# Optimization experiments

Hardware: AMD Instinct MI355X
Metric: run time of the kernel (lower is better)

## Reference

```python
import jax, jax.numpy as jnp
import numpy as np

B, T, D_MODEL, HEAD = 4, 4096, 1024, 64

def setup_inputs() -> dict:
    key = jax.random.key(0)
    ks = jax.random.split(key, 7)
    s = 0.02  # typical init scale
    return {
        "x":  jax.random.normal(ks[0], (B, T, D_MODEL), dtype=jnp.float32),
        "Wq": jax.random.normal(ks[1], (D_MODEL, HEAD), dtype=jnp.float32) * s,
        "bq": jnp.zeros((HEAD,), dtype=jnp.float32),
        "Wk": jax.random.normal(ks[2], (D_MODEL, HEAD), dtype=jnp.float32) * s,
        "bk": jnp.zeros((HEAD,), dtype=jnp.float32),
        "Wv": jax.random.normal(ks[3], (D_MODEL, HEAD), dtype=jnp.float32) * s,
        "bv": jnp.zeros((HEAD,), dtype=jnp.float32),
    }

def reference(x, Wq, bq, Wk, bk, Wv, bv):
    Bz, Tz, C = x.shape
    q = x @ Wq + bq                      # (B,T,H)
    k = x @ Wk + bk                      # (B,T,H)
    v = x @ Wv + bv                      # (B,T,H)
    # NOTE: original scales by sqrt(C) = sqrt(d_model), not sqrt(head_size)
    att = jnp.einsum("bth,bsh->bts", q, k) / jnp.sqrt(jnp.float32(C))
    causal = jnp.tril(jnp.ones((Tz, Tz), dtype=bool))
    att = jnp.where(causal, att, -jnp.inf)
    att = jax.nn.softmax(att, axis=-1)
    return jnp.einsum("bts,bsh->bth", att, v)  # (B,T,H)
```

## Files before the change

### kernel.cpp

```cpp
#include <hip/hip_runtime.h>
#include <hip/hip_bf16.h>
#include <hip/hip_fp16.h>

#define T_SEQ 4096
#define DMODEL 1024
#define HEAD 64
#define NBATCH 4
#define NSEG 544
#define S2LOG 0.04508422f

typedef __attribute__((ext_vector_type(8))) short bf16x8;
typedef __attribute__((ext_vector_type(4))) float f32x4;

__device__ __forceinline__ unsigned short f2bf(float f) {
    unsigned int b = __float_as_uint(f);
    unsigned int r = b + 0x7FFFu + ((b >> 16) & 1u);
    return (unsigned short)(r >> 16);
}
__device__ __forceinline__ unsigned int pk_bf16(float a, float b) {
    __hip_bfloat162 h = __float22bfloat162_rn(make_float2(a, b));
    unsigned int u; __builtin_memcpy(&u, &h, 4); return u;
}
__device__ __forceinline__ void dma16(const void* g, void* s) {
    __builtin_amdgcn_global_load_lds(
        (const __attribute__((address_space(1))) unsigned int*)g,
        (__attribute__((address_space(3))) unsigned int*)s, 16, 0, 0);
}

__global__ __launch_bounds__(256) void prep_w(
    const float* __restrict__ Wq, const float* __restrict__ Wk,
    const float* __restrict__ Wv, unsigned short* __restrict__ Wtb)
{
    __shared__ unsigned short tl[64 * 72];
    const int bid = blockIdx.x;
    const int m   = bid >> 4;
    const int k0  = (bid & 15) * 64;
    const float* W = (m == 0) ? Wq : (m == 1) ? Wk : Wv;
    const int t  = threadIdx.x;
    const int kr = t >> 2, qtr = t & 3;
#pragma unroll
    for (int i = 0; i < 4; ++i) {
        float4 wv4 = *(const float4*)&W[(k0 + kr) * 64 + qtr * 16 + i * 4];
        tl[(qtr * 16 + i * 4 + 0) * 72 + kr] = f2bf(wv4.x);
        tl[(qtr * 16 + i * 4 + 1) * 72 + kr] = f2bf(wv4.y);
        tl[(qtr * 16 + i * 4 + 2) * 72 + kr] = f2bf(wv4.z);
        tl[(qtr * 16 + i * 4 + 3) * 72 + kr] = f2bf(wv4.w);
    }
    __syncthreads();
#pragma unroll
    for (int c = 0; c < 2; ++c) {
        const int lin = c * 256 + t;
        const int n = lin >> 3, k8 = lin & 7;
        *(uint4*)&Wtb[((long)(m * 64 + n)) * 1024 + k0 + k8 * 8] =
            *(const uint4*)&tl[n * 72 + k8 * 8];
    }
}

__global__ __launch_bounds__(256, 3) void qkv_mfma(
    const float* __restrict__ x, const unsigned short* __restrict__ Wtb,
    const float* __restrict__ bq, const float* __restrict__ bk,
    const float* __restrict__ bv,
    unsigned short* __restrict__ qo, unsigned short* __restrict__ ko,
    unsigned short* __restrict__ vt)
{
    __shared__ __align__(16) unsigned short xs[2][4096];
    const int t    = threadIdx.x;
    const int lane = t & 63;
    const int l15  = lane & 15, quad = lane >> 4;
    const int w    = __builtin_amdgcn_readfirstlane(t >> 6);
    const long row0 = (long)blockIdx.x * 32;

    float bias[3];
#pragma unroll
    for (int ntl = 0; ntl < 3; ++ntl) {
        const int c = w * 48 + ntl * 16 + l15;
        bias[ntl] = (c < 64) ? bq[c] : (c < 128) ? bk[c - 64] : bv[c - 128];
    }
    f32x4 acc[2][3];
#pragma unroll
    for (int mt = 0; mt < 2; ++mt)
#pragma unroll
        for (int ntl = 0; ntl < 3; ++ntl)
            acc[mt][ntl] = (f32x4){bias[ntl], bias[ntl], bias[ntl], bias[ntl]};

    float4 g[4];
    auto load_stage = [&](int sg) {
#pragma unroll
        for (int s = 0; s < 4; ++s) {
            const int id = s * 256 + t, row = id >> 5, off = id & 31;
            g[s] = *(const float4*)&x[(row0 + row) * DMODEL + sg * 128 + off * 4];
        }
    };
    auto write_stage = [&](int buf) {
#pragma unroll
        for (int s = 0; s < 4; ++s) {
            const int id = s * 256 + t, row = id >> 5, off = id & 31;
            uint2 u;
            u.x = pk_bf16(g[s].x, g[s].y);
            u.y = pk_bf16(g[s].z, g[s].w);
            *(uint2*)&xs[buf][row * 128 + ((off >> 1) ^ (row & 7)) * 8 + (off & 1) * 4] = u;
        }
    };

    load_stage(0);
    write_stage(0);

    for (int sg = 0; sg < 8; ++sg) {
        __syncthreads();
        if (sg + 1 < 8) load_stage(sg + 1);
        bf16x8 wf[3][4];
#pragma unroll
        for (int ntl = 0; ntl < 3; ++ntl)
#pragma unroll
            for (int kq = 0; kq < 4; ++kq)
                wf[ntl][kq] = *(const bf16x8*)&Wtb[((long)(w * 48 + ntl * 16 + l15)) * 1024
                                                   + sg * 128 + kq * 32 + quad * 8];
#pragma unroll
        for (int mt = 0; mt < 2; ++mt)
#pragma unroll
            for (int kq = 0; kq < 4; ++kq) {
                const int row = mt * 16 + l15;
                bf16x8 a = *(const bf16x8*)&xs[sg & 1][row * 128
                                                       + ((kq * 4 + quad) ^ (row & 7)) * 8];
#pragma unroll
                for (int ntl = 0; ntl < 3; ++ntl)
                    acc[mt][ntl] = __builtin_amdgcn_mfma_f32_16x16x32_bf16(a, wf[ntl][kq], acc[mt][ntl], 0, 0, 0);
            }
        if (sg + 1 < 8) write_stage((sg + 1) & 1);
    }
#pragma unroll
    for (int mt = 0; mt < 2; ++mt)
#pragma unroll
        for (int ntl = 0; ntl < 3; ++ntl) {
            const int c = w * 48 + ntl * 16 + l15;
            const long tr0 = row0 + mt * 16 + quad * 4;
            if (c < 64) {
#pragma unroll
                for (int r = 0; r < 4; ++r)
                    qo[(tr0 + r) * HEAD + c] = f2bf(acc[mt][ntl][r] * S2LOG);
            } else if (c < 128) {
#pragma unroll
                for (int r = 0; r < 4; ++r)
                    ko[(tr0 + r) * HEAD + (c - 64)] = f2bf(acc[mt][ntl][r]);
            } else {
                const int b = (int)(tr0 >> 12), tloc = (int)(tr0 & 4095);
                uint2 pv;
                pv.x = pk_bf16(acc[mt][ntl][0], acc[mt][ntl][1]);
                pv.y = pk_bf16(acc[mt][ntl][2], acc[mt][ntl][3]);
                *(uint2*)&vt[((long)(b * HEAD + (c - 128))) * T_SEQ + tloc] = pv;
            }
        }
}

__global__ __launch_bounds__(256, 3) void flash_seg(
    const unsigned short* __restrict__ qg,
    const unsigned short* __restrict__ kg,
    const unsigned short* __restrict__ vtg,
    __half* __restrict__ opart, float* __restrict__ ml)
{
    __shared__ __align__(16) unsigned short kv_s[2][8192];
    __shared__ __align__(16) unsigned short p_s[4][16 * 72];
    const int t0   = threadIdx.x;
    const int lane = t0 & 63;
    const int l15  = lane & 15, quad = lane >> 4;
    const int wv   = __builtin_amdgcn_readfirstlane(t0 >> 6);

    const int bid = (int)blockIdx.x;
    const int sid = (NSEG - 1) - (bid >> 2);
    const int b   = bid & 3;

    int kk = 0, pref = 0;
#pragma unroll
    for (int i = 0; i < 15; ++i) {
        const int cnt = 4 * (kk + 1);
        if (sid >= pref + cnt) { pref += cnt; ++kk; }
    }
    const int S   = kk + 1;
    const int rem = sid - pref;
    const int t   = kk * 4 + rem / S;
    const int si  = rem % S;
    const int r0  = t * 64;
    const int rw  = r0 + wv * 16;
    const int nck = t + 1;
    const int c0  = (si * nck) / S, c1 = ((si + 1) * nck) / S;
    const long bbase = (long)b * T_SEQ;
    const int gidx = b * NSEG + sid;

    bf16x8 qf[2];
#pragma unroll
    for (int h = 0; h < 2; ++h)
        qf[h] = *(const bf16x8*)&qg[(bbase + rw + l15) * HEAD + h * 32 + quad * 8];

    f32x4 o[4];
#pragma unroll
    for (int dt = 0; dt < 4; ++dt) o[dt] = (f32x4){0.f, 0.f, 0.f, 0.f};
    float lrun = 0.f;
    unsigned short* ps = p_s[wv];

    auto dma_chunk = [&](int key0, int buf) {
#pragma unroll
        for (int i = 0; i < 2; ++i) {
            const int jj  = wv * 2 + i;
            const int kl  = jj * 8 + (lane >> 3);
            const int dlg = (lane & 7) ^ ((lane >> 3) & 7);
            dma16(kg + (bbase + key0 + kl) * HEAD + dlg * 8,
                  &kv_s[buf][jj * 512]);
        }
#pragma unroll
        for (int i = 0; i < 2; ++i) {
            const int jj  = wv * 2 + i;
            const int dim = jj * 8 + (lane >> 3);
            const int klg = (lane & 7) ^ ((lane >> 3) & 7);
            dma16(vtg + ((long)(b * HEAD + dim)) * T_SEQ + key0 + klg * 8,
                  &kv_s[buf][4096 + jj * 512]);
        }
    };
    dma_chunk(c0 * 64, 0);

    for (int c = c0; c < c1; ++c) {
        const int key0 = c * 64;
        const int cur  = (c - c0) & 1;
        __syncthreads();
        if (c + 1 < c1) dma_chunk((c + 1) * 64, cur ^ 1);

        f32x4 st[4];
#pragma unroll
        for (int mt = 0; mt < 4; ++mt) {
            const int key_l = mt * 16 + l15;
            bf16x8 k0 = *(const bf16x8*)&kv_s[cur][key_l * 64 + ((quad    ) ^ (l15 & 7)) * 8];
            bf16x8 k1 = *(const bf16x8*)&kv_s[cur][key_l * 64 + ((quad + 4) ^ (l15 & 7)) * 8];
            f32x4 z = (f32x4){0.f, 0.f, 0.f, 0.f};
            z = __builtin_amdgcn_mfma_f32_16x16x32_bf16(k0, qf[0], z, 0, 0, 0);
            st[mt] = __builtin_amdgcn_mfma_f32_16x16x32_bf16(k1, qf[1], st[mt] = z, 0, 0, 0);
        }
        bf16x8 vf[4][2];
#pragma unroll
        for (int dt = 0; dt < 4; ++dt) {
            const int dim = dt * 16 + l15;
            vf[dt][0] = *(const bf16x8*)&kv_s[cur][4096 + dim * 64 + ((quad    ) ^ (l15 & 7)) * 8];
            vf[dt][1] = *(const bf16x8*)&kv_s[cur][4096 + dim * 64 + ((quad + 4) ^ (l15 & 7)) * 8];
        }
        if (key0 + 63 > rw) {
            const int row = rw + l15;
#pragma unroll
            for (int mt = 0; mt < 4; ++mt)
#pragma unroll
                for (int r = 0; r < 4; ++r) {
                    const int key = key0 + mt * 16 + quad * 4 + r;
                    st[mt][r] = (key <= row) ? st[mt][r] : -30000.f;
                }
        }
        float psum = 0.f;
#pragma unroll
        for (int mt = 0; mt < 4; ++mt) {
            float e0 = exp2f(st[mt][0]), e1 = exp2f(st[mt][1]);
            float e2 = exp2f(st[mt][2]), e3 = exp2f(st[mt][3]);
            psum += (e0 + e1) + (e2 + e3);
            *(unsigned int*)&ps[l15 * 72 + mt * 16 + quad * 4]     = pk_bf16(e0, e1);
            *(unsigned int*)&ps[l15 * 72 + mt * 16 + quad * 4 + 2] = pk_bf16(e2, e3);
        }
        psum += __shfl_xor(psum, 16);
        psum += __shfl_xor(psum, 32);
        lrun += psum;
        __builtin_amdgcn_wave_barrier();
        bf16x8 pf[2];
#pragma unroll
        for (int g = 0; g < 2; ++g)
            pf[g] = *(const bf16x8*)&ps[l15 * 72 + g * 32 + quad * 8];
        __builtin_amdgcn_wave_barrier();
#pragma unroll
        for (int dt = 0; dt < 4; ++dt) {
            o[dt] = __builtin_amdgcn_mfma_f32_16x16x32_bf16(vf[dt][0], pf[0], o[dt], 0, 0, 0);
            o[dt] = __builtin_amdgcn_mfma_f32_16x16x32_bf16(vf[dt][1], pf[1], o[dt], 0, 0, 0);
        }
    }

    const float inv = (lrun > 0.f) ? 1.f / lrun : 0.f;
    __half* op = opart + (long)gidx * 4096;
#pragma unroll
    for (int dt = 0; dt < 4; ++dt) {
        __half2 h0 = __floats2half2_rn(o[dt][0] * inv, o[dt][1] * inv);
        __half2 h1 = __floats2half2_rn(o[dt][2] * inv, o[dt][3] * inv);
        uint2 u; __builtin_memcpy(&u.x, &h0, 4); __builtin_memcpy(&u.y, &h1, 4);
        *(uint2*)&op[(wv * 16 + l15) * HEAD + dt * 16 + quad * 4] = u;
    }
    if (quad == 0)
        ml[(long)gidx * 64 + wv * 16 + l15] = lrun;
}

__global__ __launch_bounds__(256) void merge_seg(
    const __half* __restrict__ opart, const float* __restrict__ ml,
    float* __restrict__ out)
{
    const int bid = blockIdx.x;
    const int half = bid & 1, t = (bid >> 1) & 63, b = bid >> 7;
    const int kk = t >> 2, S = kk + 1;
    const int base_sid = 2 * kk * (kk + 1) + (t & 3) * S;
    const int tid = threadIdx.x;
    const int row = half * 32 + (tid >> 3), col0 = (tid & 7) * 8;

    float acc[8];
#pragma unroll
    for (int j = 0; j < 8; ++j) acc[j] = 0.f;
    float L = 0.f;
    for (int si = 0; si < S; ++si) {
        const long g = (long)(b * NSEG + base_sid + si);
        const float l = ml[g * 64 + row];
        L += l;
        const __half* op = opart + g * 4096 + row * 64 + col0;
        uint4 u = *(const uint4*)op;
        __half2 h01, h23, h45, h67;
        __builtin_memcpy(&h01, &u.x, 4); __builtin_memcpy(&h23, &u.y, 4);
        __builtin_memcpy(&h45, &u.z, 4); __builtin_memcpy(&h67, &u.w, 4);
        float2 f01 = __half22float2(h01), f23 = __half22float2(h23);
        float2 f45 = __half22float2(h45), f67 = __half22float2(h67);
        acc[0] += l * f01.x; acc[1] += l * f01.y;
        acc[2] += l * f23.x; acc[3] += l * f23.y;
        acc[4] += l * f45.x; acc[5] += l * f45.y;
        acc[6] += l * f67.x; acc[7] += l * f67.y;
    }
    const float inv = 1.f / L;
    float* dst = out + ((long)(b * T_SEQ + t * 64 + row)) * HEAD + col0;
#pragma unroll
    for (int h = 0; h < 2; ++h) {
        float4 ov = {acc[h * 4] * inv, acc[h * 4 + 1] * inv,
                     acc[h * 4 + 2] * inv, acc[h * 4 + 3] * inv};
        *(float4*)(dst + h * 4) = ov;
    }
}

extern "C" void kernel_launch(void* const* d_in, const int* in_sizes, int n_in,
                              void* d_out, int out_size, void* d_ws, size_t ws_size,
                              hipStream_t stream) {
    const float* x  = (const float*)d_in[0];
    const float* Wq = (const float*)d_in[1];
    const float* bq = (const float*)d_in[2];
    const float* Wk = (const float*)d_in[3];
    const float* bk = (const float*)d_in[4];
    const float* Wv = (const float*)d_in[5];
    const float* bv = (const float*)d_in[6];
    float* outp = (float*)d_out;

    char* wsb = (char*)d_ws;
    unsigned short* wtb = (unsigned short*)(wsb);
    unsigned short* qw  = (unsigned short*)(wsb + 393216);
    unsigned short* kw  = (unsigned short*)(wsb + 2490368);
    unsigned short* vtw = (unsigned short*)(wsb + 4587520);
    __half* opart       = (__half*)(wsb + 6684672);
    float*  mlp         = (float*)(wsb + 24510464);

    prep_w<<<dim3(48), dim3(256), 0, stream>>>(Wq, Wk, Wv, wtb);
    qkv_mfma<<<dim3(512), dim3(256), 0, stream>>>(
        x, wtb, bq, bk, bv, qw, kw, vtw);
    flash_seg<<<dim3(NSEG * NBATCH), dim3(256), 0, stream>>>(qw, kw, vtw, opart, mlp);
    merge_seg<<<dim3(512), dim3(256), 0, stream>>>(opart, mlp, outp);
}
```

Measured before the change: 157.6 us.

## Stage QKV weights in LDS via async DMA and double rows per block

The projection kernel now processes 64 rows per block with 8 waves (two row groups by four column groups), so each weight tile is reused across twice as many rows. Weights are re-laid out per 128-wide k-stage and prefetched into double-buffered, swizzled LDS with global_load_lds instead of each wave reading them straight from global memory. This targets redundant global or L2 weight traffic in the QKV GEMM. In exchange it uses much more LDS per block (about 128 KB) and halves the grid to 256 blocks, which may lower occupancy.

```diff
diff --git a/kernel.cpp b/kernel.cpp
--- a/kernel.cpp
+++ b/kernel.cpp
@@ -51,29 +51,34 @@
     for (int c = 0; c < 2; ++c) {
         const int lin = c * 256 + t;
         const int n = lin >> 3, k8 = lin & 7;
-        *(uint4*)&Wtb[((long)(m * 64 + n)) * 1024 + k0 + k8 * 8] =
+        const int k = k0 + k8 * 8;
+        const int sg = k >> 7, koff = k & 127;
+        *(uint4*)&Wtb[((long)(sg * 192 + m * 64 + n)) * 128 + koff] =
             *(const uint4*)&tl[n * 72 + k8 * 8];
     }
 }
 
-__global__ __launch_bounds__(256, 3) void qkv_mfma(
+__global__ __launch_bounds__(512, 2) void qkv_mfma(
     const float* __restrict__ x, const unsigned short* __restrict__ Wtb,
     const float* __restrict__ bq, const float* __restrict__ bk,
     const float* __restrict__ bv,
     unsigned short* __restrict__ qo, unsigned short* __restrict__ ko,
     unsigned short* __restrict__ vt)
 {
-    __shared__ __align__(16) unsigned short xs[2][4096];
+    __shared__ __align__(16) unsigned short xs[2][8192];
+    __shared__ __align__(16) unsigned short wsd[2][24576];
     const int t    = threadIdx.x;
     const int lane = t & 63;
     const int l15  = lane & 15, quad = lane >> 4;
-    const int w    = __builtin_amdgcn_readfirstlane(t >> 6);
-    const long row0 = (long)blockIdx.x * 32;
+    const int wv   = __builtin_amdgcn_readfirstlane(t >> 6);
+    const int rowg = wv >> 2;
+    const int colg = wv & 3;
+    const long row0 = (long)blockIdx.x * 64;
 
     float bias[3];
 #pragma unroll
     for (int ntl = 0; ntl < 3; ++ntl) {
-        const int c = w * 48 + ntl * 16 + l15;
+        const int c = colg * 48 + ntl * 16 + l15;
         bias[ntl] = (c < 64) ? bq[c] : (c < 128) ? bk[c - 64] : bv[c - 128];
     }
     f32x4 acc[2][3];
@@ -87,39 +92,55 @@
     auto load_stage = [&](int sg) {
 #pragma unroll
         for (int s = 0; s < 4; ++s) {
-            const int id = s * 256 + t, row = id >> 5, off = id & 31;
+            const int id = s * 512 + t, row = id >> 5, off = id & 31;
             g[s] = *(const float4*)&x[(row0 + row) * DMODEL + sg * 128 + off * 4];
         }
     };
     auto write_stage = [&](int buf) {
 #pragma unroll
         for (int s = 0; s < 4; ++s) {
-            const int id = s * 256 + t, row = id >> 5, off = id & 31;
+            const int id = s * 512 + t, row = id >> 5, off = id & 31;
             uint2 u;
             u.x = pk_bf16(g[s].x, g[s].y);
             u.y = pk_bf16(g[s].z, g[s].w);
             *(uint2*)&xs[buf][row * 128 + ((off >> 1) ^ (row & 7)) * 8 + (off & 1) * 4] = u;
         }
     };
+    auto dma_w = [&](int sg, int buf) {
+#pragma unroll
+        for (int j = 0; j < 6; ++j) {
+            const int slot0 = (wv * 6 + j) * 64;
+            const int slot  = slot0 + lane;
+            const int col   = slot >> 4, ch = slot & 15;
+            dma16(Wtb + ((long)(sg * 192 + col)) * 128 + ((ch ^ (col & 7)) * 8),
+                  &wsd[buf][slot0 * 8]);
+        }
+    };
 
     load_stage(0);
+    dma_w(0, 0);
     write_stage(0);
 
     for (int sg = 0; sg < 8; ++sg) {
         __syncthreads();
-        if (sg + 1 < 8) load_stage(sg + 1);
+        if (sg + 1 < 8) {
+            load_stage(sg + 1);
+            dma_w(sg + 1, (sg + 1) & 1);
+        }
         bf16x8 wf[3][4];
 #pragma unroll
         for (int ntl = 0; ntl < 3; ++ntl)
 #pragma unroll
-            for (int kq = 0; kq < 4; ++kq)
-                wf[ntl][kq] = *(const bf16x8*)&Wtb[((long)(w * 48 + ntl * 16 + l15)) * 1024
-                                                   + sg * 128 + kq * 32 + quad * 8];
+            for (int kq = 0; kq < 4; ++kq) {
+                const int col = colg * 48 + ntl * 16 + l15;
+                wf[ntl][kq] = *(const bf16x8*)&wsd[sg & 1][col * 128
+                                                           + (((kq * 4 + quad) ^ (col & 7))) * 8];
+            }
 #pragma unroll
         for (int mt = 0; mt < 2; ++mt)
 #pragma unroll
             for (int kq = 0; kq < 4; ++kq) {
-                const int row = mt * 16 + l15;
+                const int row = rowg * 32 + mt * 16 + l15;
                 bf16x8 a = *(const bf16x8*)&xs[sg & 1][row * 128
                                                        + ((kq * 4 + quad) ^ (row & 7)) * 8];
 #pragma unroll
@@ -132,8 +153,8 @@
     for (int mt = 0; mt < 2; ++mt)
 #pragma unroll
         for (int ntl = 0; ntl < 3; ++ntl) {
-            const int c = w * 48 + ntl * 16 + l15;
-            const long tr0 = row0 + mt * 16 + quad * 4;
+            const int c = colg * 48 + ntl * 16 + l15;
+            const long tr0 = row0 + rowg * 32 + mt * 16 + quad * 4;
             if (c < 64) {
 #pragma unroll
                 for (int r = 0; r < 4; ++r)
@@ -350,7 +371,7 @@
     float*  mlp         = (float*)(wsb + 24510464);
 
     prep_w<<<dim3(48), dim3(256), 0, stream>>>(Wq, Wk, Wv, wtb);
-    qkv_mfma<<<dim3(512), dim3(256), 0, stream>>>(
+    qkv_mfma<<<dim3(256), dim3(512), 0, stream>>>(
         x, wtb, bq, bk, bv, qw, kw, vtw);
     flash_seg<<<dim3(NSEG * NBATCH), dim3(256), 0, stream>>>(qw, kw, vtw, opart, mlp);
     merge_seg<<<dim3(512), dim3(256), 0, stream>>>(opart, mlp, outp);
```

Result: faster. 147.0 us, median of 3 (-6.8%).
